# Kernel optimization log

Measured on AMD Instinct MI355X. Metric: run time of the kernel, lower is better.

Reference implementation:

```python
import jax, jax.numpy as jnp
import numpy as np

C_HID = 128   # c = int(c2 * e) = 128
N_EXP = 4
TOP_K = 2


def conv2d(x, w, b, padding='SAME'):
    # x: [B,Cin,H,W], w: [Cout,Cin,kh,kw]
    out = jax.lax.conv_general_dilated(
        x, w, window_strides=(1, 1), padding=padding,
        dimension_numbers=('NCHW', 'OIHW', 'NCHW'))
    return out + b[None, :, None, None]


def silu(x):
    return x * jax.nn.sigmoid(x)


def setup_inputs() -> dict:
    key = jax.random.key(0)
    ks = jax.random.split(key, 10)
    B, C1, H, W = 16, 256, 80, 80
    c = C_HID
    s = 0.05
    return {
        'x': jax.random.normal(ks[0], (B, C1, H, W), jnp.float32),
        'W_cv1': jax.random.normal(ks[1], (2 * c, C1, 1, 1), jnp.float32) * s,
        'b_cv1': jax.random.normal(ks[2], (2 * c,), jnp.float32) * s,
        'W_r': jax.random.normal(ks[3], (N_EXP, c), jnp.float32) * s,
        'b_r': jax.random.normal(ks[4], (N_EXP,), jnp.float32) * s,
        'W_exp': jax.random.normal(ks[5], (N_EXP, c, c, 3, 3), jnp.float32) * s,
        'b_exp': jax.random.normal(ks[6], (N_EXP, c), jnp.float32) * s,
        'W_cv2': jax.random.normal(ks[7], (256, 3 * c, 1, 1), jnp.float32) * s,
        'b_cv2': jax.random.normal(ks[8], (256,), jnp.float32) * s,
    }


def reference(x, W_cv1, b_cv1, W_r, b_r, W_exp, b_exp, W_cv2, b_cv2):
    c = C_HID
    B = x.shape[0]
    # cv1: 1x1 conv -> SiLU (BN folded into bias), split into two branches
    y = silu(conv2d(x, W_cv1, b_cv1))           # [B, 2c, H, W]
    a, m = y[:, :c], y[:, c:]                   # each [B, c, H, W]

    # CrossModalRouter: GAP -> linear -> softmax -> top-k -> renormalize
    pooled = m.mean(axis=(2, 3))                # [B, c]
    logits = pooled @ W_r.T + b_r               # [B, E]
    probs = jax.nn.softmax(logits, axis=-1)
    w, idx = jax.lax.top_k(probs, TOP_K)        # [B, k]
    w = w / w.sum(axis=-1, keepdims=True)

    # dense sparse-gate: zeros except the top-k entries
    gate = jnp.zeros((B, N_EXP), x.dtype).at[jnp.arange(B)[:, None], idx].set(w)

    # DualModalExpertContainer: E independent 3x3 conv+SiLU experts, gated sum
    exp_out = jax.vmap(lambda we, be: silu(conv2d(m, we, be)))(W_exp, b_exp)  # [E,B,c,H,W]
    moe = jnp.einsum('be,ebchw->bchw', gate, exp_out)  # [B, c, H, W]

    # cv2 over concat([y0, y1, expert_out])
    out = silu(conv2d(jnp.concatenate([a, m, moe], axis=1), W_cv2, b_cv2))
    return out
```

## Files before the change

### kernel.cpp

```cpp
#include <hip/hip_runtime.h>
#include <hip/hip_bf16.h>

#define NPIX 6400
#define IMW 80
#define IMH 80

typedef __attribute__((ext_vector_type(8))) short short8;
typedef __attribute__((ext_vector_type(4))) float floatx4;

__device__ __forceinline__ float silu_f(float v) {
    return v / (1.0f + __expf(-v));
}
__device__ __forceinline__ unsigned short f2bf(float v) {
    __hip_bfloat16 h = __float2bfloat16(v);
    return *(unsigned short*)&h;
}


__global__ __launch_bounds__(256) void prep_swz1(
    const float* __restrict__ W1, __hip_bfloat16* __restrict__ Wt1s)
{
    int t = blockIdx.x * 256 + threadIdx.x;
    int mt = t >> 9, rem = t & 511;
    int ks = rem >> 6, lane = rem & 63;
    int col = lane & 15, quad = lane >> 4;
    const float* src = W1 + (size_t)(mt * 16 + col) * 256 + ks * 32 + quad * 8;
    unsigned short pk[8];
    #pragma unroll
    for (int j = 0; j < 8; ++j) pk[j] = f2bf(src[j]);
    *(uint4*)(Wt1s + (size_t)t * 8) = *(uint4*)pk;
}

__global__ __launch_bounds__(256) void prep_swz2(
    const float* __restrict__ W2, __hip_bfloat16* __restrict__ Wt2s)
{
    int t = blockIdx.x * 256 + threadIdx.x;
    int mt = t / 768, rem = t % 768;
    int ks = rem >> 6, lane = rem & 63;
    int col = lane & 15, quad = lane >> 4;
    const float* src = W2 + (size_t)(mt * 16 + col) * 384 + ks * 32 + quad * 8;
    unsigned short pk[8];
    #pragma unroll
    for (int j = 0; j < 8; ++j) pk[j] = f2bf(src[j]);
    *(uint4*)(Wt2s + (size_t)t * 8) = *(uint4*)pk;
}

__global__ __launch_bounds__(256) void prep_swzE(
    const float* __restrict__ Wexp, __hip_bfloat16* __restrict__ Wts)
{
    int t = blockIdx.x * 256 + threadIdx.x;
    int e = t / 18432, rem = t % 18432;
    int gmt = rem / 2304, rem2 = rem % 2304;
    int s = rem2 >> 6, lane = rem2 & 63;
    int col = lane & 15, quad = lane >> 4;
    int tap = s >> 2;
    int cib = (s & 3) * 32 + quad * 8;
    int co  = gmt * 16 + col;
    const float* src = Wexp + ((size_t)(e * 128 + co) * 128 + cib) * 9 + tap;
    unsigned short pk[8];
    #pragma unroll
    for (int j = 0; j < 8; ++j) pk[j] = f2bf(src[j * 9]);
    *(uint4*)(Wts + (size_t)t * 8) = *(uint4*)pk;
}

__global__ __launch_bounds__(256) void transpose_x(
    const float* __restrict__ x, __hip_bfloat16* __restrict__ catT)
{
    const int b   = blockIdx.z;
    const int ci0 = blockIdx.y * 64;
    const int p0  = blockIdx.x * 64;
    __shared__ unsigned short t[64][70];
    const int tid = threadIdx.x;
    const float* src = x + ((size_t)b * 256 + ci0) * NPIX + p0;
    #pragma unroll
    for (int it = 0; it < 4; ++it) {
        int idx = tid + it * 256;
        int ci = idx >> 4, pg = idx & 15;
        float4 v = *(const float4*)(src + (size_t)ci * NPIX + pg * 4);
        t[pg * 4 + 0][ci] = f2bf(v.x);
        t[pg * 4 + 1][ci] = f2bf(v.y);
        t[pg * 4 + 2][ci] = f2bf(v.z);
        t[pg * 4 + 3][ci] = f2bf(v.w);
    }
    __syncthreads();
    unsigned short* dst = (unsigned short*)catT + ((size_t)b * NPIX + p0) * 384 + ci0;
    #pragma unroll
    for (int it = 0; it < 2; ++it) {
        int idx = tid + it * 256;
        int p = idx >> 3, cg = idx & 7;
        unsigned short vv[8];
        #pragma unroll
        for (int j = 0; j < 8; ++j) vv[j] = t[p][cg * 8 + j];
        *(uint4*)(dst + (size_t)p * 384 + cg * 8) = *(uint4*)vv;
    }
}

__global__ __launch_bounds__(256, 2) void cv1_mfma(
    const __hip_bfloat16* __restrict__ Wt1s, const float* __restrict__ b1,
    __hip_bfloat16* __restrict__ catT, float* __restrict__ pooled)
{
    const int b  = blockIdx.y;
    const int p0 = blockIdx.x * 128;
    const int tid = threadIdx.x;
    const int wave = tid >> 6, lane = tid & 63;
    const int col = lane & 15, quad = lane >> 4;
    const int cohalf  = (wave & 1) * 128;
    const int gmt0    = (wave & 1) * 8;
    const int pixhalf = (wave >> 1) * 64;

    __hip_bfloat16* ct = catT + (size_t)b * NPIX * 384;
    int pp[4];
    #pragma unroll
    for (int nt = 0; nt < 4; ++nt) pp[nt] = p0 + pixhalf + nt * 16 + col;

    floatx4 acc[8][4] = {};

    #pragma unroll
    for (int ks = 0; ks < 8; ++ks) {
        short8 bf[4];
        #pragma unroll
        for (int nt = 0; nt < 4; ++nt)
            bf[nt] = *(const short8*)&ct[(size_t)pp[nt] * 384 + ks * 32 + quad * 8];
        #pragma unroll
        for (int mt = 0; mt < 8; ++mt) {
            short8 af = *(const short8*)&Wt1s[(size_t)(((gmt0 + mt) * 8 + ks) * 64 + lane) * 8];
            #pragma unroll
            for (int nt = 0; nt < 4; ++nt)
                acc[mt][nt] = __builtin_amdgcn_mfma_f32_16x16x32_bf16(af, bf[nt], acc[mt][nt], 0, 0, 0);
        }
    }

    __syncthreads();

    #pragma unroll
    for (int mt = 0; mt < 8; ++mt) {
        const int cobase = cohalf + mt * 16 + quad * 4;
        float bias[4];
        #pragma unroll
        for (int r = 0; r < 4; ++r) bias[r] = b1[cobase + r];
        float v[4][4];
        #pragma unroll
        for (int nt = 0; nt < 4; ++nt) {
            unsigned short pk[4];
            #pragma unroll
            for (int r = 0; r < 4; ++r) {
                v[nt][r] = silu_f(acc[mt][nt][r] + bias[r]);
                pk[r] = f2bf(v[nt][r]);
            }
            *(uint2*)&ct[(size_t)pp[nt] * 384 + cobase] = *(uint2*)pk;
        }
        if (cohalf == 128) {
            #pragma unroll
            for (int r = 0; r < 4; ++r) {
                float s = v[0][r] + v[1][r] + v[2][r] + v[3][r];
                #pragma unroll
                for (int m = 1; m < 16; m <<= 1)
                    s += __shfl_xor(s, m, 64);
                if (col == 0)
                    atomicAdd(&pooled[b * 128 + (cobase - 128) + r], s * (1.0f / NPIX));
            }
        }
    }
}

__global__ __launch_bounds__(64) void router_kernel(
    const float* __restrict__ pooled, const float* __restrict__ Wr,
    const float* __restrict__ br, int* __restrict__ sel_idx, float* __restrict__ sel_w)
{
    __shared__ float lg[16][4];
    int tid = threadIdx.x;
    int b = tid >> 2, e = tid & 3;
    float s = br[e];
    for (int c2 = 0; c2 < 128; c2++)
        s += pooled[b * 128 + c2] * Wr[e * 128 + c2];
    lg[b][e] = s;
    __syncthreads();
    if (tid < 16) {
        int bb = tid;
        float l[4]; float mx = -1e30f;
        #pragma unroll
        for (int i = 0; i < 4; i++) { l[i] = lg[bb][i]; mx = fmaxf(mx, l[i]); }
        float p[4]; float sum = 0.f;
        #pragma unroll
        for (int i = 0; i < 4; i++) { p[i] = __expf(l[i] - mx); sum += p[i]; }
        #pragma unroll
        for (int i = 0; i < 4; i++) p[i] /= sum;
        int i1 = 0;
        for (int i = 1; i < 4; i++) if (p[i] > p[i1]) i1 = i;
        int i2 = (i1 == 0) ? 1 : 0;
        for (int i = 0; i < 4; i++) if (i != i1 && p[i] > p[i2]) i2 = i;
        float inv = 1.0f / (p[i1] + p[i2]);
        sel_idx[bb * 2 + 0] = i1; sel_idx[bb * 2 + 1] = i2;
        sel_w[bb * 2 + 0] = p[i1] * inv; sel_w[bb * 2 + 1] = p[i2] * inv;
    }
}

__global__ __launch_bounds__(256, 2) void expert_gemm(
    __hip_bfloat16* __restrict__ catT, const __hip_bfloat16* __restrict__ Wts,
    const float* __restrict__ bexp, const int* __restrict__ sel_idx,
    const float* __restrict__ sel_w)
{
    const int b  = blockIdx.y;
    const int p0 = blockIdx.x * 128;
    const int e0 = sel_idx[b * 2 + 0], e1 = sel_idx[b * 2 + 1];
    const float g0 = sel_w[b * 2 + 0], g1 = sel_w[b * 2 + 1];

    const int tid  = threadIdx.x;
    const int wave = tid >> 6, lane = tid & 63;
    const int col  = lane & 15, quad = lane >> 4;
    const int cohalf  = (wave & 1) * 64;
    const int gmt0    = (wave & 1) * 4;
    const int pixhalf = (wave >> 1) * 64;

    __hip_bfloat16* ct = catT + (size_t)b * NPIX * 384;
    const __hip_bfloat16* wsrc[2];
    wsrc[0] = Wts + (size_t)e0 * 8 * 36 * 64 * 8 + (size_t)lane * 8;
    wsrc[1] = Wts + (size_t)e1 * 8 * 36 * 64 * 8 + (size_t)lane * 8;

    int pp[4], prow[4], pcol[4];
    #pragma unroll
    for (int nt = 0; nt < 4; ++nt) {
        pp[nt]   = p0 + pixhalf + nt * 16 + col;
        prow[nt] = pp[nt] / IMW;
        pcol[nt] = pp[nt] % IMW;
    }

    floatx4 acc[2][4][4] = {};

    for (int tap = 0; tap < 9; ++tap) {
        const int dyy = tap / 3 - 1, dxx = tap % 3 - 1;
        bool valid[4];
        const __hip_bfloat16* bbase[4];
        #pragma unroll
        for (int nt = 0; nt < 4; ++nt) {
            int ir = prow[nt] + dyy, ic = pcol[nt] + dxx;
            valid[nt] = ((unsigned)ir < IMH) && ((unsigned)ic < IMW);
            bbase[nt] = ct + (size_t)(ir * IMW + ic) * 384 + 128 + quad * 8;
        }
        #pragma unroll
        for (int ss = 0; ss < 4; ++ss) {
            const int s = tap * 4 + ss;
            short8 bf[4];
            #pragma unroll
            for (int nt = 0; nt < 4; ++nt) {
                int4 vv = {0, 0, 0, 0};
                if (valid[nt]) vv = *(const int4*)(bbase[nt] + ss * 32);
                bf[nt] = *(short8*)&vv;
            }
            #pragma unroll
            for (int e = 0; e < 2; ++e) {
                #pragma unroll
                for (int mt = 0; mt < 4; ++mt) {
                    short8 af = *(const short8*)(wsrc[e] + (size_t)((gmt0 + mt) * 36 + s) * 64 * 8);
                    #pragma unroll
                    for (int nt = 0; nt < 4; ++nt)
                        acc[e][mt][nt] = __builtin_amdgcn_mfma_f32_16x16x32_bf16(
                            af, bf[nt], acc[e][mt][nt], 0, 0, 0);
                }
            }
        }
    }

    #pragma unroll
    for (int mt = 0; mt < 4; ++mt) {
        const int cobase = cohalf + mt * 16 + quad * 4;
        #pragma unroll
        for (int nt = 0; nt < 4; ++nt) {
            unsigned short pk[4];
            #pragma unroll
            for (int r = 0; r < 4; ++r) {
                int coo = cobase + r;
                float vb0 = bexp[e0 * 128 + coo];
                float vb1 = bexp[e1 * 128 + coo];
                float v = g0 * silu_f(acc[0][mt][nt][r] + vb0)
                        + g1 * silu_f(acc[1][mt][nt][r] + vb1);
                pk[r] = f2bf(v);
            }
            *(uint2*)&ct[(size_t)pp[nt] * 384 + 256 + cobase] = *(uint2*)pk;
        }
    }
}

__global__ __launch_bounds__(256, 2) void cv2_mfma(
    const __hip_bfloat16* __restrict__ catT, const __hip_bfloat16* __restrict__ Wt2s,
    const float* __restrict__ b2, float* __restrict__ out)
{
    const int b  = blockIdx.y;
    const int p0 = blockIdx.x * 128;
    const int tid = threadIdx.x;
    const int wave = tid >> 6, lane = tid & 63;
    const int col = lane & 15, quad = lane >> 4;
    const int cohalf  = (wave & 1) * 128;
    const int gmt0    = (wave & 1) * 8;
    const int pixhalf = (wave >> 1) * 64;

    const __hip_bfloat16* ct = catT + (size_t)b * NPIX * 384;
    int pp[4];
    #pragma unroll
    for (int nt = 0; nt < 4; ++nt) pp[nt] = p0 + pixhalf + nt * 16 + col;

    floatx4 acc[8][4] = {};

    #pragma unroll
    for (int ks = 0; ks < 12; ++ks) {
        short8 bf[4];
        #pragma unroll
        for (int nt = 0; nt < 4; ++nt)
            bf[nt] = *(const short8*)&ct[(size_t)pp[nt] * 384 + ks * 32 + quad * 8];
        #pragma unroll
        for (int mt = 0; mt < 8; ++mt) {
            short8 af = *(const short8*)&Wt2s[(size_t)(((gmt0 + mt) * 12 + ks) * 64 + lane) * 8];
            #pragma unroll
            for (int nt = 0; nt < 4; ++nt)
                acc[mt][nt] = __builtin_amdgcn_mfma_f32_16x16x32_bf16(af, bf[nt], acc[mt][nt], 0, 0, 0);
        }
    }

    #pragma unroll
    for (int mt = 0; mt < 8; ++mt) {
        const int cobase = cohalf + mt * 16 + quad * 4;
        #pragma unroll
        for (int r = 0; r < 4; ++r) {
            float bias = b2[cobase + r];
            size_t rowb = ((size_t)b * 256 + cobase + r) * NPIX;
            #pragma unroll
            for (int nt = 0; nt < 4; ++nt)
                out[rowb + pp[nt]] = silu_f(acc[mt][nt][r] + bias);
        }
    }
}

extern "C" void kernel_launch(void* const* d_in, const int* in_sizes, int n_in,
                              void* d_out, int out_size, void* d_ws, size_t ws_size,
                              hipStream_t stream)
{
    (void)in_sizes; (void)n_in; (void)out_size; (void)ws_size;
    const float* x    = (const float*)d_in[0];
    const float* W1   = (const float*)d_in[1];
    const float* b1   = (const float*)d_in[2];
    const float* Wr   = (const float*)d_in[3];
    const float* br   = (const float*)d_in[4];
    const float* Wexp = (const float*)d_in[5];
    const float* bexp = (const float*)d_in[6];
    const float* W2   = (const float*)d_in[7];
    const float* b2   = (const float*)d_in[8];
    float* out = (float*)d_out;

    char* ws = (char*)d_ws;
    __hip_bfloat16* catT = (__hip_bfloat16*)ws;
    __hip_bfloat16* Wts  = (__hip_bfloat16*)(ws + 78643200);
    __hip_bfloat16* Wt1s = (__hip_bfloat16*)(ws + 79822848);
    __hip_bfloat16* Wt2s = (__hip_bfloat16*)(ws + 79953920);
    float* pooled        = (float*)(ws + 80150528);
    int*   sel_idx       = (int*)(ws + 80158720);
    float* sel_w         = (float*)(ws + 80158848);

    hipMemsetAsync(pooled, 0, 16 * 128 * 4, stream);
    prep_swz1    <<<dim3(32),         256, 0, stream>>>(W1, Wt1s);
    prep_swz2    <<<dim3(48),         256, 0, stream>>>(W2, Wt2s);
    prep_swzE    <<<dim3(288),        256, 0, stream>>>(Wexp, Wts);
    transpose_x  <<<dim3(100, 4, 16), 256, 0, stream>>>(x, catT);
    cv1_mfma     <<<dim3(50, 16),     256, 0, stream>>>(Wt1s, b1, catT, pooled);
    router_kernel<<<1,                 64, 0, stream>>>(pooled, Wr, br, sel_idx, sel_w);
    expert_gemm  <<<dim3(50, 16),     256, 0, stream>>>(catT, Wts, bexp, sel_idx, sel_w);
    cv2_mfma     <<<dim3(50, 16),     256, 0, stream>>>(catT, Wt2s, b2, out);
}
```

Before: 475.5 us.

## Stage expert conv input halo rows in swizzled LDS, tile by image rows

```diff
diff --git a/kernel.cpp b/kernel.cpp
--- a/kernel.cpp
+++ b/kernel.cpp
@@ -200,83 +200,95 @@
     const float* __restrict__ bexp, const int* __restrict__ sel_idx,
     const float* __restrict__ sel_w)
 {
-    const int b  = blockIdx.y;
-    const int p0 = blockIdx.x * 128;
+    __shared__ __align__(16) unsigned char smem[4 * 82 * 128];
+    const int b = blockIdx.y;
+    const int y = blockIdx.x;
     const int e0 = sel_idx[b * 2 + 0], e1 = sel_idx[b * 2 + 1];
     const float g0 = sel_w[b * 2 + 0], g1 = sel_w[b * 2 + 1];
 
     const int tid  = threadIdx.x;
     const int wave = tid >> 6, lane = tid & 63;
     const int col  = lane & 15, quad = lane >> 4;
-    const int cohalf  = (wave & 1) * 64;
-    const int gmt0    = (wave & 1) * 4;
-    const int pixhalf = (wave >> 1) * 64;
+    const int cohalf = (wave & 1) * 64;
+    const int gmt0   = (wave & 1) * 4;
+    const int pixh   = wave >> 1;
 
     __hip_bfloat16* ct = catT + (size_t)b * NPIX * 384;
     const __hip_bfloat16* wsrc[2];
-    wsrc[0] = Wts + (size_t)e0 * 8 * 36 * 64 * 8 + (size_t)lane * 8;
-    wsrc[1] = Wts + (size_t)e1 * 8 * 36 * 64 * 8 + (size_t)lane * 8;
-
-    int pp[4], prow[4], pcol[4];
-    #pragma unroll
-    for (int nt = 0; nt < 4; ++nt) {
-        pp[nt]   = p0 + pixhalf + nt * 16 + col;
-        prow[nt] = pp[nt] / IMW;
-        pcol[nt] = pp[nt] % IMW;
-    }
-
-    floatx4 acc[2][4][4] = {};
-
-    for (int tap = 0; tap < 9; ++tap) {
-        const int dyy = tap / 3 - 1, dxx = tap % 3 - 1;
-        bool valid[4];
-        const __hip_bfloat16* bbase[4];
-        #pragma unroll
-        for (int nt = 0; nt < 4; ++nt) {
-            int ir = prow[nt] + dyy, ic = pcol[nt] + dxx;
-            valid[nt] = ((unsigned)ir < IMH) && ((unsigned)ic < IMW);
-            bbase[nt] = ct + (size_t)(ir * IMW + ic) * 384 + 128 + quad * 8;
-        }
-        #pragma unroll
-        for (int ss = 0; ss < 4; ++ss) {
-            const int s = tap * 4 + ss;
-            short8 bf[4];
-            #pragma unroll
-            for (int nt = 0; nt < 4; ++nt) {
-                int4 vv = {0, 0, 0, 0};
-                if (valid[nt]) vv = *(const int4*)(bbase[nt] + ss * 32);
-                bf[nt] = *(short8*)&vv;
-            }
-            #pragma unroll
-            for (int e = 0; e < 2; ++e) {
+    wsrc[0] = Wts + (size_t)e0 * (8 * 36 * 64 * 8) + (size_t)lane * 8;
+    wsrc[1] = Wts + (size_t)e1 * (8 * 36 * 64 * 8) + (size_t)lane * 8;
+
+    floatx4 acc[2][4][5] = {};
+    const int rbase = y * 2;
+
+    for (int cib = 0; cib < 2; ++cib) {
+        if (cib) __syncthreads();
+        #pragma unroll
+        for (int k = 0; k < 11; ++k) {
+            int i = k * 256 + tid;
+            if (i < 4 * 82 * 8) {
+                int pix_l = i >> 3, sl = i & 7;
+                int rowl = pix_l / 82, pcl = pix_l % 82;
+                int r_img = rbase - 1 + rowl;
+                int c_img = pcl - 1;
+                int4 v = {0, 0, 0, 0};
+                if ((unsigned)r_img < (unsigned)IMH && (unsigned)c_img < (unsigned)IMW)
+                    v = *(const int4*)(ct + (size_t)(r_img * IMW + c_img) * 384
+                                       + 128 + cib * 64 + sl * 8);
+                *(int4*)(smem + rowl * (82 * 128) + pcl * 128
+                         + ((sl ^ (pcl & 7)) * 16)) = v;
+            }
+        }
+        __syncthreads();
+
+        #pragma unroll
+        for (int tap = 0; tap < 9; ++tap) {
+            const int dy = tap / 3;
+            const int dx = tap % 3 - 1;
+            const int rowl = pixh + dy;
+            #pragma unroll
+            for (int ks = 0; ks < 2; ++ks) {
+                const int s = tap * 4 + cib * 2 + ks;
+                short8 bf[5];
                 #pragma unroll
-                for (int mt = 0; mt < 4; ++mt) {
-                    short8 af = *(const short8*)(wsrc[e] + (size_t)((gmt0 + mt) * 36 + s) * 64 * 8);
+                for (int nt = 0; nt < 5; ++nt) {
+                    int pcl = nt * 16 + col + dx + 1;
+                    int sl  = (ks * 4 + quad) ^ (pcl & 7);
+                    bf[nt] = *(const short8*)(smem + rowl * (82 * 128)
+                                              + pcl * 128 + sl * 16);
+                }
+                #pragma unroll
+                for (int e = 0; e < 2; ++e) {
                     #pragma unroll
-                    for (int nt = 0; nt < 4; ++nt)
-                        acc[e][mt][nt] = __builtin_amdgcn_mfma_f32_16x16x32_bf16(
-                            af, bf[nt], acc[e][mt][nt], 0, 0, 0);
+                    for (int mt = 0; mt < 4; ++mt) {
+                        short8 af = *(const short8*)(wsrc[e]
+                                     + (size_t)((gmt0 + mt) * 36 + s) * 64 * 8);
+                        #pragma unroll
+                        for (int nt = 0; nt < 5; ++nt)
+                            acc[e][mt][nt] = __builtin_amdgcn_mfma_f32_16x16x32_bf16(
+                                af, bf[nt], acc[e][mt][nt], 0, 0, 0);
+                    }
                 }
             }
         }
     }
 
+    const int prow = rbase + pixh;
     #pragma unroll
     for (int mt = 0; mt < 4; ++mt) {
         const int cobase = cohalf + mt * 16 + quad * 4;
         #pragma unroll
-        for (int nt = 0; nt < 4; ++nt) {
+        for (int nt = 0; nt < 5; ++nt) {
+            int pix = prow * IMW + nt * 16 + col;
             unsigned short pk[4];
             #pragma unroll
             for (int r = 0; r < 4; ++r) {
                 int coo = cobase + r;
-                float vb0 = bexp[e0 * 128 + coo];
-                float vb1 = bexp[e1 * 128 + coo];
-                float v = g0 * silu_f(acc[0][mt][nt][r] + vb0)
-                        + g1 * silu_f(acc[1][mt][nt][r] + vb1);
+                float v = g0 * silu_f(acc[0][mt][nt][r] + bexp[e0 * 128 + coo])
+                        + g1 * silu_f(acc[1][mt][nt][r] + bexp[e1 * 128 + coo]);
                 pk[r] = f2bf(v);
             }
-            *(uint2*)&ct[(size_t)pp[nt] * 384 + 256 + cobase] = *(uint2*)pk;
+            *(uint2*)&ct[(size_t)pix * 384 + 256 + cobase] = *(uint2*)pk;
         }
     }
 }
@@ -362,6 +374,6 @@
     transpose_x  <<<dim3(100, 4, 16), 256, 0, stream>>>(x, catT);
     cv1_mfma     <<<dim3(50, 16),     256, 0, stream>>>(Wt1s, b1, catT, pooled);
     router_kernel<<<1,                 64, 0, stream>>>(pooled, Wr, br, sel_idx, sel_w);
-    expert_gemm  <<<dim3(50, 16),     256, 0, stream>>>(catT, Wts, bexp, sel_idx, sel_w);
+    expert_gemm  <<<dim3(40, 16),     256, 0, stream>>>(catT, Wts, bexp, sel_idx, sel_w);
     cv2_mfma     <<<dim3(50, 16),     256, 0, stream>>>(catT, Wt2s, b2, out);
 }
```

Measured after the change: 609.5 us. 1.28x slower.
